# Kernel optimization log

Hardware: AMD Instinct MI355X
Metric: run time of the kernel (lower is better)

The kernel has to match this reference:

```python
import jax, jax.numpy as jnp
import numpy as np

B = 4          # graphs
N = 8192       # coarse nodes (2048/graph)
M = 65536      # fine (skip) nodes (16384/graph)
E = 131072     # edges (32768/graph)
T = 16         # global tokens per graph
F_IN = 16      # dim of x and x_skip (concat -> in_channels = 32)
HID, OUT = 32, 16
ED, GD, EMB, H = 3, 1024, 64, 4
K = 3


def _make_pe(t, d):
    # PositionalEncoding buffer (sin/cos), deterministic constant
    position = np.arange(t, dtype=np.float32)[:, None]
    div = np.exp(np.arange(0, d, 2, dtype=np.float32) * (-np.log(10000.0) / d))
    pe = np.zeros((t, d), dtype=np.float32)
    pe[:, 0::2] = np.sin(position * div)
    pe[:, 1::2] = np.cos(position * div)
    return jnp.asarray(pe)


def setup_inputs():
    key = jax.random.key(0)
    ks = jax.random.split(key, 30)
    n, m, e = N // B, M // B, E // B
    inp = {}
    inp['x'] = jax.random.normal(ks[0], (N, F_IN), jnp.float32)
    inp['pos'] = jax.random.normal(ks[1], (N, 3), jnp.float32)
    inp['batch'] = jnp.repeat(jnp.arange(B), n)
    inp['x_skip'] = jax.random.normal(ks[2], (M, F_IN), jnp.float32)
    inp['pos_skip'] = jax.random.normal(ks[3], (M, 3), jnp.float32)
    inp['batch_skip'] = jnp.repeat(jnp.arange(B), m)
    off = jnp.repeat(jnp.arange(B) * m, e)
    inp['edge_index'] = jax.random.randint(ks[4], (2, E), 0, m) + off[None, :]
    inp['global_token'] = jax.random.normal(ks[5], (B * T, GD), jnp.float32)
    def lin(k, o, i, s):
        return jax.random.normal(k, (o, i), jnp.float32) * s
    inp['Wq_w'] = lin(ks[6], EMB, ED, 0.3); inp['Wq_b'] = jnp.zeros((EMB,), jnp.float32)
    inp['Wk_w'] = lin(ks[7], EMB, GD, 0.03); inp['Wk_b'] = jnp.zeros((EMB,), jnp.float32)
    inp['Wv_w'] = lin(ks[8], EMB, GD, 0.03); inp['Wv_b'] = jnp.zeros((EMB,), jnp.float32)
    inp['in_proj_w'] = lin(ks[9], 3 * EMB, EMB, 0.125); inp['in_proj_b'] = jnp.zeros((3 * EMB,), jnp.float32)
    inp['out_w'] = lin(ks[10], EMB, EMB, 0.125); inp['out_b'] = jnp.zeros((EMB,), jnp.float32)
    dims = [(2 * F_IN, HID), (HID, HID), (HID, OUT)]
    for i, (ci, co) in enumerate(dims):
        inp[f'nn_w{i}'] = lin(ks[11 + 3 * i], ci * co, ED + EMB, 0.05)
        inp[f'nn_b{i}'] = jnp.zeros((ci * co,), jnp.float32)
        inp[f'root{i}'] = jax.random.normal(ks[12 + 3 * i], (ci, co), jnp.float32) * (1.0 / np.sqrt(ci))
        inp[f'bias{i}'] = jnp.zeros((co,), jnp.float32)
    return inp


def reference(x, pos, batch, x_skip, pos_skip, batch_skip, edge_index, global_token,
              Wq_w, Wq_b, Wk_w, Wk_b, Wv_w, Wv_b, in_proj_w, in_proj_b, out_w, out_b,
              nn_w0, nn_b0, root0, bias0, nn_w1, nn_b1, root1, bias1, nn_w2, nn_b2, root2, bias2):
    # ---- knn_interpolate (k=3, inverse squared-distance weighting) ----
    # graphs are equal-sized by construction so per-graph knn == batched knn
    pos_b = pos.reshape(B, -1, 3)
    posk_b = pos_skip.reshape(B, -1, 3)
    d2 = ((posk_b ** 2).sum(-1)[:, :, None] + (pos_b ** 2).sum(-1)[:, None, :]
          - 2.0 * jnp.einsum('bmc,bnc->bmn', posk_b, pos_b))  # [B,m,n]
    neg, idx = jax.lax.top_k(-d2, K)                           # [B,m,K]
    w = 1.0 / jnp.maximum(-neg, 1e-16)
    x_b = x.reshape(B, -1, x.shape[-1])
    feats = jnp.take_along_axis(x_b[:, None, :, :], idx[:, :, :, None], axis=2)  # [B,m,K,F]
    xf = ((w[..., None] * feats).sum(2) / w.sum(2)[..., None]).reshape(M, -1)

    src, dst = edge_index[0], edge_index[1]
    pseudo = pos_skip[dst] - pos_skip[src]                     # patch_size is None
    edge_pos = (0.5 * (pos_skip[dst] + pos_skip[src])).reshape(B, -1, 3)
    gt = global_token.reshape(B, -1, global_token.shape[-1])
    pe = _make_pe(gt.shape[1], EMB)
    Q = edge_pos @ Wq_w.T + Wq_b                               # [B,Eb,EMB]
    Kt = gt @ Wk_w.T + Wk_b + pe                               # dropout in eval = identity
    Vt = gt @ Wv_w.T + Wv_b + pe
    # ---- MultiheadAttention (batch_first) ----
    wq, wk, wv = jnp.split(in_proj_w, 3, axis=0)
    bq, bk, bv = jnp.split(in_proj_b, 3, axis=0)
    hd = EMB // H
    def heads(t, w_, b_):
        t = t @ w_.T + b_
        return t.reshape(t.shape[0], t.shape[1], H, hd).transpose(0, 2, 1, 3)
    q, k_, v = heads(Q, wq, bq), heads(Kt, wk, bk), heads(Vt, wv, bv)
    att = jax.nn.softmax(jnp.einsum('bhqd,bhkd->bhqk', q, k_) / np.sqrt(hd).astype(np.float32), axis=-1)
    o = jnp.einsum('bhqk,bhkd->bhqd', att, v).transpose(0, 2, 1, 3).reshape(B, -1, EMB)
    o = o @ out_w.T + out_b
    pseudo = jnp.concatenate([pseudo, o.reshape(-1, EMB)], axis=-1)  # [E, 3+64]

    # ---- NNConv stack (gather -> edge MLP -> per-edge matmul -> scatter mean) ----
    h = jnp.concatenate([xf, x_skip], axis=1)                  # [M, 32]
    ones = jnp.ones((E,), jnp.float32)
    cnt = jnp.maximum(jax.ops.segment_sum(ones, dst, num_segments=M), 1.0)[:, None]
    for nw, nb, rt, bs in ((nn_w0, nn_b0, root0, bias0),
                           (nn_w1, nn_b1, root1, bias1),
                           (nn_w2, nn_b2, root2, bias2)):
        ci, co = rt.shape
        we = jax.nn.relu(pseudo @ nw.T + nb).reshape(E, ci, co)  # MLP (BN at default eval stats ~ identity)
        msg = jnp.einsum('ei,eio->eo', h[src], we)               # [E, co]
        aggr = jax.ops.segment_sum(msg, dst, num_segments=M) / cnt
        h = jax.nn.relu(aggr + h @ rt + bs)                      # drop_act=False -> relu every layer
    return h, pos_skip, batch_skip
```

## Files before the change

### kernel.cpp

```cpp
#include <hip/hip_runtime.h>
#include <math.h>

#define NB    4
#define NN    8192
#define MM    65536
#define EE    131072
#define NPG   2048

typedef short short8 __attribute__((ext_vector_type(8)));
typedef float f32x4  __attribute__((ext_vector_type(4)));

static __device__ inline unsigned short f2b(float f) {
    unsigned u = __float_as_uint(f);
    u += 0x7fffu + ((u >> 16) & 1u);
    return (unsigned short)(u >> 16);
}
static __device__ inline unsigned f2b_pack(float a, float b) {
    unsigned x = __float_as_uint(a); x += 0x7fffu + ((x >> 16) & 1u);
    unsigned y = __float_as_uint(b); y += 0x7fffu + ((y >> 16) & 1u);
    return (x >> 16) | (y & 0xffff0000u);
}
static __device__ inline short8 bc8(uint4 v) {
    union { uint4 u; short8 s; } c; c.u = v; return c.s;
}

__global__ __launch_bounds__(512)
void k_knn(const float4* __restrict__ cpre, const float* __restrict__ pos_skip,
           const float* __restrict__ x, const float* __restrict__ x_skip,
           const int* __restrict__ batch_skip,
           float* __restrict__ h0, float* __restrict__ out_pos,
           float* __restrict__ out_batch)
{
    __shared__ float4 cp[2048];
    __shared__ float  pk[8][128][3];
    __shared__ int    chosen[128][3];
    __shared__ unsigned long long fin[3][128][3];
    __shared__ float  wFin[128][3];
    __shared__ int    iFin[128][3];

    int tid = threadIdx.x;
    int g = blockIdx.x >> 7;
    int cbase = g * NPG;
    int fbase = blockIdx.x * 128;
    int wave = tid >> 6;
    int lane = tid & 63;

    for (int c = tid; c < 2048; c += 512) cp[c] = cpre[cbase + c];

    int nA = lane, nB = lane + 64;
    float fxA = pos_skip[(fbase + nA) * 3 + 0];
    float fyA = pos_skip[(fbase + nA) * 3 + 1];
    float fzA = pos_skip[(fbase + nA) * 3 + 2];
    float fxB = pos_skip[(fbase + nB) * 3 + 0];
    float fyB = pos_skip[(fbase + nB) * 3 + 1];
    float fzB = pos_skip[(fbase + nB) * 3 + 2];
    __syncthreads();

    const float4* cps = cp + wave * 256;
    float k0A = 3.4028235e38f, k1A = 3.4028235e38f, k2A = 3.4028235e38f;
    float k0B = 3.4028235e38f, k1B = 3.4028235e38f, k2B = 3.4028235e38f;
#pragma unroll
    for (int j = 0; j < 8; ++j) {
        float mA = 3.4028235e38f, mB = 3.4028235e38f;
#pragma unroll 8
        for (int i = 0; i < 32; ++i) {
            float4 cc = cps[j * 32 + i];
            float dA = fmaf(cc.x, fxA, cc.w);
            dA = fmaf(cc.y, fyA, dA);
            dA = fmaf(cc.z, fzA, dA);
            mA = fminf(mA, dA);
            float dB = fmaf(cc.x, fxB, cc.w);
            dB = fmaf(cc.y, fyB, dB);
            dB = fmaf(cc.z, fzB, dB);
            mB = fminf(mB, dB);
        }
        unsigned cid = (unsigned)(wave * 8 + j);
        float keyA = __uint_as_float((__float_as_uint(mA) & 0xFFFFFFC0u) | cid);
        float tA = fmaxf(k1A, keyA);
        k2A = fminf(k2A, tA);
        k1A = __builtin_amdgcn_fmed3f(k0A, k1A, keyA);
        k0A = fminf(k0A, keyA);
        float keyB = __uint_as_float((__float_as_uint(mB) & 0xFFFFFFC0u) | cid);
        float tB = fmaxf(k1B, keyB);
        k2B = fminf(k2B, tB);
        k1B = __builtin_amdgcn_fmed3f(k0B, k1B, keyB);
        k0B = fminf(k0B, keyB);
    }
    pk[wave][nA][0] = k0A; pk[wave][nA][1] = k1A; pk[wave][nA][2] = k2A;
    pk[wave][nB][0] = k0B; pk[wave][nB][1] = k1B; pk[wave][nB][2] = k2B;
    __syncthreads();

    if (tid < 128) {
        int n = tid;
        float m0 = 3.4028235e38f, m1 = 3.4028235e38f, m2 = 3.4028235e38f;
#pragma unroll
        for (int s = 0; s < 8; ++s)
#pragma unroll
            for (int r = 0; r < 3; ++r) {
                float k = pk[s][n][r];
                float t = fmaxf(m1, k);
                m2 = fminf(m2, t);
                m1 = __builtin_amdgcn_fmed3f(m0, m1, k);
                m0 = fminf(m0, k);
            }
        chosen[n][0] = (int)(__float_as_uint(m0) & 63u);
        chosen[n][1] = (int)(__float_as_uint(m1) & 63u);
        chosen[n][2] = (int)(__float_as_uint(m2) & 63u);
    }
    __syncthreads();

    if ((tid >> 7) < 3) {
        int n = tid & 127;
        int j = tid >> 7;
        int cid = chosen[n][j];
        int fn = fbase + n;
        float gx = pos_skip[fn * 3 + 0], gy = pos_skip[fn * 3 + 1], gz = pos_skip[fn * 3 + 2];
        float gq = gx * gx + gy * gy + gz * gz;
        unsigned long long m0 = ~0ull, m1 = ~0ull, m2 = ~0ull;
#pragma unroll 4
        for (int i = 0; i < 32; ++i) {
            int ii = (i + lane) & 31;
            float4 cc = cp[cid * 32 + ii];
            float d = gq + cc.w;
            d = fmaf(cc.x, gx, d);
            d = fmaf(cc.y, gy, d);
            d = fmaf(cc.z, gz, d);
            d = fmaxf(d, 0.f);
            unsigned c = (unsigned)(cbase + cid * 32 + ii);
            unsigned long long kk = ((unsigned long long)__float_as_uint(d) << 32) | c;
            unsigned long long t1 = m0 > kk ? m0 : kk; m0 = m0 < kk ? m0 : kk;
            unsigned long long t2 = m1 > t1 ? m1 : t1; m1 = m1 < t1 ? m1 : t1;
            m2 = m2 < t2 ? m2 : t2;
        }
        fin[j][n][0] = m0; fin[j][n][1] = m1; fin[j][n][2] = m2;
    }
    __syncthreads();

    if (tid < 128) {
        int n = tid;
        int fn = fbase + n;
        unsigned long long m0 = ~0ull, m1 = ~0ull, m2 = ~0ull;
#pragma unroll
        for (int j = 0; j < 3; ++j)
#pragma unroll
            for (int r = 0; r < 3; ++r) {
                unsigned long long kk = fin[j][n][r];
                unsigned long long t1 = m0 > kk ? m0 : kk; m0 = m0 < kk ? m0 : kk;
                unsigned long long t2 = m1 > t1 ? m1 : t1; m1 = m1 < t1 ? m1 : t1;
                m2 = m2 < t2 ? m2 : t2;
            }
        float d0 = __uint_as_float((unsigned)(m0 >> 32));
        float d1 = __uint_as_float((unsigned)(m1 >> 32));
        float d2 = __uint_as_float((unsigned)(m2 >> 32));
        float w0 = 1.f / fmaxf(d0, 1e-16f);
        float w1 = 1.f / fmaxf(d1, 1e-16f);
        float w2 = 1.f / fmaxf(d2, 1e-16f);
        float inv = 1.f / (w0 + w1 + w2);
        wFin[n][0] = w0 * inv; wFin[n][1] = w1 * inv; wFin[n][2] = w2 * inv;
        iFin[n][0] = (int)(m0 & 0xffffffffull);
        iFin[n][1] = (int)(m1 & 0xffffffffull);
        iFin[n][2] = (int)(m2 & 0xffffffffull);
        float gx = pos_skip[fn * 3 + 0], gy = pos_skip[fn * 3 + 1], gz = pos_skip[fn * 3 + 2];
        out_pos[fn * 3 + 0] = gx; out_pos[fn * 3 + 1] = gy; out_pos[fn * 3 + 2] = gz;
        out_batch[fn] = (float)batch_skip[fn];
    }
    __syncthreads();

    int n2 = tid >> 2, part = tid & 3;
    int f2 = fbase + n2;
    float4* h04 = (float4*)(h0 + (size_t)f2 * 32);
    if (part < 2) {
        const float4* x4 = (const float4*)x;
        float w0 = wFin[n2][0], w1 = wFin[n2][1], w2 = wFin[n2][2];
        int a0 = iFin[n2][0] * 4, a1 = iFin[n2][1] * 4, a2 = iFin[n2][2] * 4;
#pragma unroll
        for (int j = 0; j < 2; ++j) {
            int cj = part * 2 + j;
            float4 v0 = x4[a0 + cj], v1 = x4[a1 + cj], v2 = x4[a2 + cj];
            float4 r;
            r.x = w0 * v0.x + w1 * v1.x + w2 * v2.x;
            r.y = w0 * v0.y + w1 * v1.y + w2 * v2.y;
            r.z = w0 * v0.z + w1 * v1.z + w2 * v2.z;
            r.w = w0 * v0.w + w1 * v1.w + w2 * v2.w;
            h04[cj] = r;
        }
    } else {
        const float4* xs4 = (const float4*)x_skip;
#pragma unroll
        for (int j = 0; j < 2; ++j) {
            int cj = (part - 2) * 2 + j;
            h04[4 + cj] = xs4[f2 * 4 + cj];
        }
    }
}

__global__ __launch_bounds__(128)
void k_tokens1(const float* __restrict__ gt,
               const float* __restrict__ Wk_w, const float* __restrict__ Wk_b,
               const float* __restrict__ Wv_w, const float* __restrict__ Wv_b,
               const float* __restrict__ pos, float4* __restrict__ cpre,
               float* __restrict__ KtVt)
{
    int cgid = blockIdx.x * 128 + threadIdx.x;
    {
        float px = pos[cgid * 3 + 0];
        float py = pos[cgid * 3 + 1];
        float pz = pos[cgid * 3 + 2];
        cpre[cgid] = make_float4(-2.f * px, -2.f * py, -2.f * pz,
                                 px * px + py * py + pz * pz);
    }
    int b = blockIdx.x >> 4;
    int t = blockIdx.x & 15;
    int which = threadIdx.x >> 6;
    int d = threadIdx.x & 63;
    const float* W = which ? Wv_w : Wk_w;
    const float* bias = which ? Wv_b : Wk_b;
    const float4* row = (const float4*)(gt + (size_t)(b * 16 + t) * 1024);
    const float4* wr = (const float4*)(W + (size_t)d * 1024);
    float acc = 0.f;
    for (int c = 0; c < 256; ++c) {
        float4 a = row[c], w = wr[c];
        acc += a.x * w.x; acc += a.y * w.y; acc += a.z * w.z; acc += a.w * w.w;
    }
    int i2 = d >> 1;
    float dv = expf((float)(2 * i2) * (-0.14391156831212787f));
    float ang = (float)t * dv;
    float pe = (d & 1) ? cosf(ang) : sinf(ang);
    KtVt[((size_t)(b * 2 + which) * 16 + t) * 64 + d] = acc + bias[d] + pe;
}

__global__ __launch_bounds__(256)
void k_tokens2(const float* __restrict__ KtVt,
               const float* __restrict__ in_proj_w, const float* __restrict__ in_proj_b,
               const float* __restrict__ out_w,
               const float* __restrict__ Wq_w, const float* __restrict__ Wq_b,
               float* __restrict__ Mfold, uint4* __restrict__ v2fG)
{
    int b = blockIdx.x;
    int tid = threadIdx.x;
    __shared__ float KtL[1024], VtL[1024], vv[1024], kproj[1024];
    __shared__ float v2L[4096];
    __shared__ float qWs[192], qbs[64];
    for (int idx = tid; idx < 1024; idx += 256) {
        KtL[idx] = KtVt[(size_t)(b * 2 + 0) * 1024 + idx];
        VtL[idx] = KtVt[(size_t)(b * 2 + 1) * 1024 + idx];
    }
    __syncthreads();
    for (int idx = tid; idx < 2048; idx += 256) {
        int which = idx >> 10; int td = idx & 1023; int t = td >> 6; int j = td & 63;
        int r = (which ? 128 : 64) + j;
        const float* w = in_proj_w + (size_t)r * 64;
        const float* src = which ? VtL : KtL;
        float acc = in_proj_b[r];
#pragma unroll 8
        for (int dd = 0; dd < 64; ++dd) acc += src[t * 64 + dd] * w[dd];
        if (which) vv[t * 64 + j] = acc;
        else kproj[t * 64 + j] = acc;
    }
    for (int idx = tid; idx < 192; idx += 256) {
        int c = idx >> 6; int j = idx & 63;
        float acc = 0.f;
        for (int dd = 0; dd < 64; ++dd) acc += in_proj_w[(size_t)j * 64 + dd] * Wq_w[dd * 3 + c];
        qWs[c * 64 + j] = acc;
    }
    for (int j = tid; j < 64; j += 256) {
        float acc = in_proj_b[j];
        for (int dd = 0; dd < 64; ++dd) acc += in_proj_w[(size_t)j * 64 + dd] * Wq_b[dd];
        qbs[j] = acc;
    }
    __syncthreads();
    for (int idx = tid; idx < 4096; idx += 256) {
        int jo = idx & 63; int th2 = idx >> 6; int h = th2 & 3; int t = th2 >> 2;
        float acc = 0.f;
#pragma unroll
        for (int dd = 0; dd < 16; ++dd)
            acc += vv[t * 64 + h * 16 + dd] * out_w[(size_t)jo * 64 + h * 16 + dd];
        v2L[(t * 4 + h) * 64 + jo] = acc;
    }
    {
        int th = tid >> 2, c = tid & 3;
        int t = th >> 2, h = th & 3;
        float acc = 0.f;
#pragma unroll
        for (int dd = h * 16; dd < h * 16 + 16; ++dd) {
            float w = (c == 0) ? qWs[dd] : (c == 1) ? qWs[64 + dd]
                    : (c == 2) ? qWs[128 + dd] : qbs[dd];
            acc += w * kproj[t * 64 + dd];
        }
        Mfold[((size_t)b * 64 + th) * 4 + c] = 0.25f * acc;
    }
    __syncthreads();
    for (int it = tid; it < 512; it += 256) {
        int lane = it & 63, fi = it >> 6;
        int mi = fi >> 1, step = fi & 1;
        int outd = mi * 16 + (lane & 15);
        int th0 = step * 32 + (lane >> 4) * 8;
        uint4 v;
        v.x = f2b_pack(v2L[(th0 + 0) * 64 + outd], v2L[(th0 + 1) * 64 + outd]);
        v.y = f2b_pack(v2L[(th0 + 2) * 64 + outd], v2L[(th0 + 3) * 64 + outd]);
        v.z = f2b_pack(v2L[(th0 + 4) * 64 + outd], v2L[(th0 + 5) * 64 + outd]);
        v.w = f2b_pack(v2L[(th0 + 6) * 64 + outd], v2L[(th0 + 7) * 64 + outd]);
        v2fG[((size_t)b * 8 + fi) * 64 + lane] = v;
    }
}

__global__ __launch_bounds__(256)
void k_edge_attn(const float* __restrict__ ps, const int* __restrict__ ei,
                 const float* __restrict__ Mfold, const uint4* __restrict__ v2f,
                 const float* __restrict__ ob,
                 unsigned short* __restrict__ Pf, float* __restrict__ cnt)
{
    __shared__ unsigned attL[4 * 64 * 34];
    int tid = threadIdx.x;
    int wave = tid >> 6, lane = tid & 63, q = lane >> 4, c15 = lane & 15;
    int g = blockIdx.x >> 7;
    int e = blockIdx.x * 256 + tid;
    int s = ei[e], d = ei[EE + e];
    atomicAdd(&cnt[d], 1.f);
    float sx = ps[s * 3], sy = ps[s * 3 + 1], sz = ps[s * 3 + 2];
    float dx = ps[d * 3], dy = ps[d * 3 + 1], dz = ps[d * 3 + 2];
    float px = dx - sx, py = dy - sy, pz = dz - sz;
    float ex = 0.5f * (dx + sx), ey = 0.5f * (dy + sy), ez = 0.5f * (dz + sz);

    const float4* Mg = (const float4*)Mfold + (size_t)g * 64;
    float sc[64];
#pragma unroll
    for (int th = 0; th < 64; ++th) {
        float4 m = Mg[th];
        sc[th] = ex * m.x + ey * m.y + ez * m.z + m.w;
    }
#pragma unroll
    for (int h = 0; h < 4; ++h) {
        float mx = sc[h];
#pragma unroll
        for (int t = 1; t < 16; ++t) mx = fmaxf(mx, sc[t * 4 + h]);
        float ssum = 0.f;
#pragma unroll
        for (int t = 0; t < 16; ++t) {
            float eo = expf(sc[t * 4 + h] - mx);
            sc[t * 4 + h] = eo; ssum += eo;
        }
        float inv = 1.f / ssum;
#pragma unroll
        for (int t = 0; t < 16; ++t) sc[t * 4 + h] *= inv;
    }
    unsigned* slab = attL + wave * 64 * 34;
#pragma unroll
    for (int k = 0; k < 16; ++k) {
        uint2 v;
        v.x = f2b_pack(sc[4 * k + 0], sc[4 * k + 1]);
        v.y = f2b_pack(sc[4 * k + 2], sc[4 * k + 3]);
        *(uint2*)&slab[lane * 34 + 2 * k] = v;
    }
    __syncthreads();

    uint4 v2a[4][2];
#pragma unroll
    for (int mi = 0; mi < 4; ++mi)
#pragma unroll
        for (int st = 0; st < 2; ++st)
            v2a[mi][st] = v2f[((size_t)g * 8 + mi * 2 + st) * 64 + lane];

    f32x4 acc[4][4];
#pragma unroll
    for (int mi = 0; mi < 4; ++mi)
#pragma unroll
        for (int nt = 0; nt < 4; ++nt) acc[mi][nt] = (f32x4){0.f, 0.f, 0.f, 0.f};

#pragma unroll
    for (int nt = 0; nt < 4; ++nt) {
        const unsigned* rb = &slab[(nt * 16 + c15) * 34];
        uint4 b0 = *(const uint4*)&rb[q * 4];
        uint4 b1 = *(const uint4*)&rb[16 + q * 4];
#pragma unroll
        for (int mi = 0; mi < 4; ++mi) {
            acc[mi][nt] = __builtin_amdgcn_mfma_f32_16x16x32_bf16(bc8(v2a[mi][0]), bc8(b0), acc[mi][nt], 0, 0, 0);
            acc[mi][nt] = __builtin_amdgcn_mfma_f32_16x16x32_bf16(bc8(v2a[mi][1]), bc8(b1), acc[mi][nt], 0, 0, 0);
        }
    }
    __syncthreads();

    float4 obv[4];
#pragma unroll
    for (int mi = 0; mi < 4; ++mi) obv[mi] = *(const float4*)(ob + mi * 16 + q * 4);
#pragma unroll
    for (int mi = 0; mi < 4; ++mi)
#pragma unroll
        for (int nt = 0; nt < 4; ++nt) {
            f32x4 a = acc[mi][nt];
            uint2 v;
            v.x = f2b_pack(a[0] + obv[mi].x, a[1] + obv[mi].y);
            v.y = f2b_pack(a[2] + obv[mi].z, a[3] + obv[mi].w);
            *(uint2*)&slab[(nt * 16 + c15) * 34 + mi * 8 + q * 2] = v;
        }
    __syncthreads();

    uint4* Pf4 = (uint4*)Pf;
#pragma unroll
    for (int et = 0; et < 4; ++et) {
        int etg = blockIdx.x * 16 + wave * 4 + et;
#pragma unroll
        for (int st = 0; st < 2; ++st) {
            uint4 w = *(const uint4*)&slab[(et * 16 + c15) * 34 + st * 16 + q * 4];
            Pf4[((size_t)etg * 3 + st) * 64 + lane] = w;
        }
    }
    int et2 = e >> 4, eL = e & 15;
    size_t tb = ((size_t)(et2 * 3 + 2) * 64 + 0 * 16 + eL) * 8;
    uint2 t0; t0.x = f2b_pack(px, py); t0.y = f2b_pack(pz, 1.0f);
    *(uint2*)(Pf + tb) = t0;
    uint2 z2; z2.x = 0u; z2.y = 0u;
    *(uint2*)(Pf + tb + 4) = z2;
#pragma unroll
    for (int quad = 1; quad < 4; ++quad) {
        size_t zb = ((size_t)(et2 * 3 + 2) * 64 + quad * 16 + eL) * 8;
        uint4 z4; z4.x = 0u; z4.y = 0u; z4.z = 0u; z4.w = 0u;
        *(uint4*)(Pf + zb) = z4;
    }
}

static __device__ inline void repack_one(const float* __restrict__ nw,
                                         const float* __restrict__ nb,
                                         unsigned short* __restrict__ Wf, int idx)
{
    int jj = idx & 7;
    int lane = (idx >> 3) & 63;
    int rest = idx >> 9;
    int s = rest % 3;
    int jt = rest / 3;
    int j = jt * 16 + (lane & 15);
    int k = s * 32 + (lane >> 4) * 8 + jj;
    float v;
    if (k < 64)       v = nw[(size_t)j * 67 + 3 + k];
    else if (k < 67)  v = nw[(size_t)j * 67 + (k - 64)];
    else if (k == 67) v = nb[j];
    else              v = 0.f;
    Wf[idx] = f2b(v);
}

__global__ __launch_bounds__(256)
void k_repackAll(const float* __restrict__ nw0, const float* __restrict__ nb0,
                 const float* __restrict__ nw1, const float* __restrict__ nb1,
                 const float* __restrict__ nw2, const float* __restrict__ nb2,
                 unsigned short* __restrict__ Wf0, unsigned short* __restrict__ Wf1,
                 unsigned short* __restrict__ Wf2)
{
    int idx = blockIdx.x * 256 + threadIdx.x;
    if (idx < 98304)        repack_one(nw0, nb0, Wf0, idx);
    else if (idx < 196608)  repack_one(nw1, nb1, Wf1, idx - 98304);
    else                    repack_one(nw2, nb2, Wf2, idx - 196608);
}

template<int CO>
__global__ __launch_bounds__(256, 4)
void k_conv_mfma(const uint4* __restrict__ Pf, const float* __restrict__ hin,
                 const int* __restrict__ ei, const uint4* __restrict__ Wf,
                 float* __restrict__ aggr)
{
    __shared__ float hL[128 * 36];
    __shared__ int sL[128];
    __shared__ int dL[128];
    constexpr int REDSZ = (CO == 16) ? 2 * 64 * 17 : 4;
    __shared__ float red[REDSZ];

    int tid = threadIdx.x;
    int e0 = blockIdx.x * 128;
    if (tid < 128) sL[tid] = ei[e0 + tid];
    else           dL[tid - 128] = ei[EE + e0 + (tid - 128)];
    __syncthreads();
    for (int idx = tid; idx < 1024; idx += 256) {
        int row = idx >> 3, c = idx & 7;
        const float4* hr = (const float4*)(hin + (size_t)sL[row] * 32);
        *(float4*)&hL[row * 36 + c * 4] = hr[c];
    }
    __syncthreads();

    int wave = tid >> 6, lane = tid & 63, quad = lane >> 4, col = lane & 15;
    int group = wave >> 1, half = wave & 1;

    uint4 a[4][3];
    int et0 = blockIdx.x * 8 + group * 4;
#pragma unroll
    for (int st = 0; st < 4; ++st)
#pragma unroll
        for (int s = 0; s < 3; ++s)
            a[st][s] = Pf[((size_t)(et0 + st) * 3 + s) * 64 + lane];

    float msg[4][4];
#pragma unroll
    for (int st = 0; st < 4; ++st)
#pragma unroll
        for (int r = 0; r < 4; ++r) msg[st][r] = 0.f;

    int ibase = (CO == 32) ? 0 : half * 16;
    constexpr int NI2 = (CO == 32) ? 16 : 8;

    for (int i2 = 0; i2 < NI2; ++i2) {
        float2 hv2[4][4];
#pragma unroll
        for (int st = 0; st < 4; ++st)
#pragma unroll
            for (int r = 0; r < 4; ++r)
                hv2[st][r] = *(const float2*)&hL[(group * 64 + st * 16 + quad * 4 + r) * 36
                                                 + ibase + i2 * 2];
#pragma unroll
        for (int ii = 0; ii < 2; ++ii) {
            int i = ibase + i2 * 2 + ii;
            int jt = (CO == 32) ? (i * 2 + half) : i;
            uint4 b0 = Wf[((size_t)jt * 3 + 0) * 64 + lane];
            uint4 b1 = Wf[((size_t)jt * 3 + 1) * 64 + lane];
            uint4 b2 = Wf[((size_t)jt * 3 + 2) * 64 + lane];
#pragma unroll
            for (int st = 0; st < 4; ++st) {
                f32x4 c = {0.f, 0.f, 0.f, 0.f};
                c = __builtin_amdgcn_mfma_f32_16x16x32_bf16(bc8(a[st][0]), bc8(b0), c, 0, 0, 0);
                c = __builtin_amdgcn_mfma_f32_16x16x32_bf16(bc8(a[st][1]), bc8(b1), c, 0, 0, 0);
                c = __builtin_amdgcn_mfma_f32_16x16x32_bf16(bc8(a[st][2]), bc8(b2), c, 0, 0, 0);
#pragma unroll
                for (int r = 0; r < 4; ++r) {
                    float hv = ii ? hv2[st][r].y : hv2[st][r].x;
                    msg[st][r] += hv * fmaxf(c[r], 0.f);
                }
            }
        }
    }

    if (CO == 32) {
#pragma unroll
        for (int st = 0; st < 4; ++st)
#pragma unroll
            for (int r = 0; r < 4; ++r) {
                int dv = dL[group * 64 + st * 16 + quad * 4 + r];
                atomicAdd(&aggr[(size_t)dv * 32 + half * 16 + col], msg[st][r]);
            }
    } else {
        if (half == 1) {
#pragma unroll
            for (int st = 0; st < 4; ++st)
#pragma unroll
                for (int r = 0; r < 4; ++r)
                    red[group * 64 * 17 + lane * 17 + st * 4 + r] = msg[st][r];
        }
        __syncthreads();
        if (half == 0) {
#pragma unroll
            for (int st = 0; st < 4; ++st)
#pragma unroll
                for (int r = 0; r < 4; ++r) {
                    float m = msg[st][r] + red[group * 64 * 17 + lane * 17 + st * 4 + r];
                    int dv = dL[group * 64 + st * 16 + quad * 4 + r];
                    atomicAdd(&aggr[(size_t)dv * 16 + col], m);
                }
        }
    }
}

template<int CO>
__global__ __launch_bounds__(256)
void k_update(float* __restrict__ aggr, const float* __restrict__ cnt,
              const float* __restrict__ hin, const float* __restrict__ root,
              const float* __restrict__ bias, float* __restrict__ hout)
{
    __shared__ float rL[32 * CO];
    __shared__ float bL[CO];
    int tid = threadIdx.x;
    for (int idx = tid; idx < 32 * CO; idx += 256) rL[idx] = root[idx];
    if (tid < CO) bL[tid] = bias[tid];
    __syncthreads();
    int gid = blockIdx.x * 256 + tid;
    int v = gid / CO;
    int o = gid % CO;
    float acc = aggr[gid] / fmaxf(cnt[v], 1.f) + bL[o];
    aggr[gid] = 0.f;
    const float* hr = hin + (size_t)v * 32;
#pragma unroll
    for (int i = 0; i < 32; ++i) acc += hr[i] * rL[i * CO + o];
    hout[gid] = fmaxf(acc, 0.f);
}

extern "C" void kernel_launch(void* const* d_in, const int* in_sizes, int n_in,
                              void* d_out, int out_size, void* d_ws, size_t ws_size,
                              hipStream_t stream)
{
    const float* x          = (const float*)d_in[0];
    const float* pos        = (const float*)d_in[1];
    const float* x_skip     = (const float*)d_in[3];
    const float* pos_skip   = (const float*)d_in[4];
    const int*   batch_skip = (const int*)  d_in[5];
    const int*   ei         = (const int*)  d_in[6];
    const float* gt         = (const float*)d_in[7];
    const float* Wq_w       = (const float*)d_in[8];
    const float* Wq_b       = (const float*)d_in[9];
    const float* Wk_w       = (const float*)d_in[10];
    const float* Wk_b       = (const float*)d_in[11];
    const float* Wv_w       = (const float*)d_in[12];
    const float* Wv_b       = (const float*)d_in[13];
    const float* in_proj_w  = (const float*)d_in[14];
    const float* in_proj_b  = (const float*)d_in[15];
    const float* out_w      = (const float*)d_in[16];
    const float* out_b      = (const float*)d_in[17];
    const float* nn_w0 = (const float*)d_in[18]; const float* nn_b0 = (const float*)d_in[19];
    const float* root0 = (const float*)d_in[20]; const float* bias0 = (const float*)d_in[21];
    const float* nn_w1 = (const float*)d_in[22]; const float* nn_b1 = (const float*)d_in[23];
    const float* root1 = (const float*)d_in[24]; const float* bias1 = (const float*)d_in[25];
    const float* nn_w2 = (const float*)d_in[26]; const float* nn_b2 = (const float*)d_in[27];
    const float* root2 = (const float*)d_in[28]; const float* bias2 = (const float*)d_in[29];

    char* wsb = (char*)d_ws;
    size_t off = 0;
    auto carve = [&](size_t bytes) { char* p = wsb + off; off += (bytes + 255) & ~(size_t)255; return p; };
    float* aggr = (float*)carve((size_t)MM * 32 * 4);
    float* cnt  = (float*)carve((size_t)MM * 4);
    float* hA   = (float*)carve((size_t)MM * 32 * 4);
    float* hB   = (float*)carve((size_t)MM * 32 * 4);
    unsigned short* Pf  = (unsigned short*)carve((size_t)EE * 96 * 2);
    unsigned short* Wf0 = (unsigned short*)carve((size_t)1024 * 96 * 2);
    unsigned short* Wf1 = (unsigned short*)carve((size_t)1024 * 96 * 2);
    unsigned short* Wf2 = (unsigned short*)carve((size_t)512 * 96 * 2);
    float* Mfold = (float*)carve((size_t)NB * 64 * 4 * 4);
    uint4* v2f   = (uint4*)carve((size_t)NB * 8 * 64 * 16);
    float* KtVt  = (float*)carve((size_t)NB * 2 * 16 * 64 * 4);
    float4* cpre = (float4*)carve((size_t)NN * 16);

    float* h_final   = (float*)d_out;
    float* out_pos   = (float*)d_out + (size_t)MM * 16;
    float* out_batch = (float*)d_out + (size_t)MM * 19;

    hipMemsetAsync(aggr, 0, ((size_t)MM * 32 + MM) * sizeof(float), stream);

    k_tokens1<<<64, 128, 0, stream>>>(gt, Wk_w, Wk_b, Wv_w, Wv_b, pos, cpre, KtVt);
    k_tokens2<<<NB, 256, 0, stream>>>(KtVt, in_proj_w, in_proj_b, out_w, Wq_w, Wq_b,
                                      Mfold, v2f);
    k_knn<<<MM / 128, 512, 0, stream>>>(cpre, pos_skip, x, x_skip, batch_skip,
                                        hA, out_pos, out_batch);
    k_edge_attn<<<EE / 256, 256, 0, stream>>>(pos_skip, ei, Mfold, v2f, out_b,
                                              Pf, cnt);
    k_repackAll<<<960, 256, 0, stream>>>(nn_w0, nn_b0, nn_w1, nn_b1, nn_w2, nn_b2,
                                         Wf0, Wf1, Wf2);

    k_conv_mfma<32><<<EE / 128, 256, 0, stream>>>((const uint4*)Pf, hA, ei, (const uint4*)Wf0, aggr);
    k_update<32><<<(MM * 32) / 256, 256, 0, stream>>>(aggr, cnt, hA, root0, bias0, hB);
    k_conv_mfma<32><<<EE / 128, 256, 0, stream>>>((const uint4*)Pf, hB, ei, (const uint4*)Wf1, aggr);
    k_update<32><<<(MM * 32) / 256, 256, 0, stream>>>(aggr, cnt, hB, root1, bias1, hA);
    k_conv_mfma<16><<<EE / 128, 256, 0, stream>>>((const uint4*)Pf, hA, ei, (const uint4*)Wf2, aggr);
    k_update<16><<<(MM * 16) / 256, 256, 0, stream>>>(aggr, cnt, hA, root2, bias2, h_final);
}
```

Measured before the change: 345.8 us.

## Transpose gathered node features in LDS and compute kNN prep inline

Result: slower. 354.1 us (+2.4%).

```diff
diff --git a/kernel.cpp b/kernel.cpp
--- a/kernel.cpp
+++ b/kernel.cpp
@@ -9,6 +9,7 @@
 
 typedef short short8 __attribute__((ext_vector_type(8)));
 typedef float f32x4  __attribute__((ext_vector_type(4)));
+typedef float f32x2  __attribute__((ext_vector_type(2)));
 
 static __device__ inline unsigned short f2b(float f) {
     unsigned u = __float_as_uint(f);
@@ -25,7 +26,7 @@
 }
 
 __global__ __launch_bounds__(512)
-void k_knn(const float4* __restrict__ cpre, const float* __restrict__ pos_skip,
+void k_knn(const float* __restrict__ pos, const float* __restrict__ pos_skip,
            const float* __restrict__ x, const float* __restrict__ x_skip,
            const int* __restrict__ batch_skip,
            float* __restrict__ h0, float* __restrict__ out_pos,
@@ -45,7 +46,14 @@
     int wave = tid >> 6;
     int lane = tid & 63;
 
-    for (int c = tid; c < 2048; c += 512) cp[c] = cpre[cbase + c];
+    for (int c = tid; c < 2048; c += 512) {
+        int cc = cbase + c;
+        float px = pos[cc * 3 + 0];
+        float py = pos[cc * 3 + 1];
+        float pz = pos[cc * 3 + 2];
+        cp[c] = make_float4(-2.f * px, -2.f * py, -2.f * pz,
+                            px * px + py * py + pz * pz);
+    }
 
     int nA = lane, nB = lane + 64;
     float fxA = pos_skip[(fbase + nA) * 3 + 0];
@@ -198,17 +206,8 @@
 void k_tokens1(const float* __restrict__ gt,
                const float* __restrict__ Wk_w, const float* __restrict__ Wk_b,
                const float* __restrict__ Wv_w, const float* __restrict__ Wv_b,
-               const float* __restrict__ pos, float4* __restrict__ cpre,
                float* __restrict__ KtVt)
 {
-    int cgid = blockIdx.x * 128 + threadIdx.x;
-    {
-        float px = pos[cgid * 3 + 0];
-        float py = pos[cgid * 3 + 1];
-        float pz = pos[cgid * 3 + 2];
-        cpre[cgid] = make_float4(-2.f * px, -2.f * py, -2.f * pz,
-                                 px * px + py * py + pz * pz);
-    }
     int b = blockIdx.x >> 4;
     int t = blockIdx.x & 15;
     int which = threadIdx.x >> 6;
@@ -457,7 +456,7 @@
                  const int* __restrict__ ei, const uint4* __restrict__ Wf,
                  float* __restrict__ aggr)
 {
-    __shared__ float hL[128 * 36];
+    __shared__ float hT[32 * 130];
     __shared__ int sL[128];
     __shared__ int dL[128];
     constexpr int REDSZ = (CO == 16) ? 2 * 64 * 17 : 4;
@@ -471,7 +470,11 @@
     for (int idx = tid; idx < 1024; idx += 256) {
         int row = idx >> 3, c = idx & 7;
         const float4* hr = (const float4*)(hin + (size_t)sL[row] * 32);
-        *(float4*)&hL[row * 36 + c * 4] = hr[c];
+        float4 v = hr[c];
+        hT[(c * 4 + 0) * 130 + row] = v.x;
+        hT[(c * 4 + 1) * 130 + row] = v.y;
+        hT[(c * 4 + 2) * 130 + row] = v.z;
+        hT[(c * 4 + 3) * 130 + row] = v.w;
     }
     __syncthreads();
 
@@ -486,71 +489,74 @@
         for (int s = 0; s < 3; ++s)
             a[st][s] = Pf[((size_t)(et0 + st) * 3 + s) * 64 + lane];
 
-    float msg[4][4];
-#pragma unroll
-    for (int st = 0; st < 4; ++st)
-#pragma unroll
-        for (int r = 0; r < 4; ++r) msg[st][r] = 0.f;
-
+    f32x2 msg[4][2];
+#pragma unroll
+    for (int st = 0; st < 4; ++st) {
+        msg[st][0] = (f32x2){0.f, 0.f};
+        msg[st][1] = (f32x2){0.f, 0.f};
+    }
+
+    int rowb = group * 64 + quad * 4;
     int ibase = (CO == 32) ? 0 : half * 16;
-    constexpr int NI2 = (CO == 32) ? 16 : 8;
-
-    for (int i2 = 0; i2 < NI2; ++i2) {
-        float2 hv2[4][4];
+    constexpr int NI = (CO == 32) ? 32 : 16;
+
+#pragma unroll 2
+    for (int io = 0; io < NI; ++io) {
+        int i = ibase + io;
+        int jt = (CO == 32) ? (i * 2 + half) : i;
+        uint4 b0 = Wf[((size_t)jt * 3 + 0) * 64 + lane];
+        uint4 b1 = Wf[((size_t)jt * 3 + 1) * 64 + lane];
+        uint4 b2 = Wf[((size_t)jt * 3 + 2) * 64 + lane];
+        const float* hTi = &hT[i * 130 + rowb];
+#pragma unroll
+        for (int st = 0; st < 4; ++st) {
+            f32x4 c4 = {0.f, 0.f, 0.f, 0.f};
+            c4 = __builtin_amdgcn_mfma_f32_16x16x32_bf16(bc8(a[st][0]), bc8(b0), c4, 0, 0, 0);
+            c4 = __builtin_amdgcn_mfma_f32_16x16x32_bf16(bc8(a[st][1]), bc8(b1), c4, 0, 0, 0);
+            c4 = __builtin_amdgcn_mfma_f32_16x16x32_bf16(bc8(a[st][2]), bc8(b2), c4, 0, 0, 0);
+            f32x2 h01 = *(const f32x2*)&hTi[st * 16 + 0];
+            f32x2 h23 = *(const f32x2*)&hTi[st * 16 + 2];
+            f32x2 r01; r01[0] = fmaxf(c4[0], 0.f); r01[1] = fmaxf(c4[1], 0.f);
+            f32x2 r23; r23[0] = fmaxf(c4[2], 0.f); r23[1] = fmaxf(c4[3], 0.f);
+            msg[st][0] += h01 * r01;
+            msg[st][1] += h23 * r23;
+        }
+    }
+
+    if (CO == 32) {
 #pragma unroll
         for (int st = 0; st < 4; ++st)
 #pragma unroll
-            for (int r = 0; r < 4; ++r)
-                hv2[st][r] = *(const float2*)&hL[(group * 64 + st * 16 + quad * 4 + r) * 36
-                                                 + ibase + i2 * 2];
-#pragma unroll
-        for (int ii = 0; ii < 2; ++ii) {
-            int i = ibase + i2 * 2 + ii;
-            int jt = (CO == 32) ? (i * 2 + half) : i;
-            uint4 b0 = Wf[((size_t)jt * 3 + 0) * 64 + lane];
-            uint4 b1 = Wf[((size_t)jt * 3 + 1) * 64 + lane];
-            uint4 b2 = Wf[((size_t)jt * 3 + 2) * 64 + lane];
-#pragma unroll
-            for (int st = 0; st < 4; ++st) {
-                f32x4 c = {0.f, 0.f, 0.f, 0.f};
-                c = __builtin_amdgcn_mfma_f32_16x16x32_bf16(bc8(a[st][0]), bc8(b0), c, 0, 0, 0);
-                c = __builtin_amdgcn_mfma_f32_16x16x32_bf16(bc8(a[st][1]), bc8(b1), c, 0, 0, 0);
-                c = __builtin_amdgcn_mfma_f32_16x16x32_bf16(bc8(a[st][2]), bc8(b2), c, 0, 0, 0);
-#pragma unroll
-                for (int r = 0; r < 4; ++r) {
-                    float hv = ii ? hv2[st][r].y : hv2[st][r].x;
-                    msg[st][r] += hv * fmaxf(c[r], 0.f);
+            for (int p = 0; p < 2; ++p)
+#pragma unroll
+                for (int e2 = 0; e2 < 2; ++e2) {
+                    int r = p * 2 + e2;
+                    int dv = dL[group * 64 + st * 16 + quad * 4 + r];
+                    atomicAdd(&aggr[(size_t)dv * 32 + half * 16 + col], msg[st][p][e2]);
                 }
-            }
-        }
-    }
-
-    if (CO == 32) {
-#pragma unroll
-        for (int st = 0; st < 4; ++st)
-#pragma unroll
-            for (int r = 0; r < 4; ++r) {
-                int dv = dL[group * 64 + st * 16 + quad * 4 + r];
-                atomicAdd(&aggr[(size_t)dv * 32 + half * 16 + col], msg[st][r]);
-            }
     } else {
         if (half == 1) {
 #pragma unroll
             for (int st = 0; st < 4; ++st)
 #pragma unroll
-                for (int r = 0; r < 4; ++r)
-                    red[group * 64 * 17 + lane * 17 + st * 4 + r] = msg[st][r];
+                for (int p = 0; p < 2; ++p)
+#pragma unroll
+                    for (int e2 = 0; e2 < 2; ++e2)
+                        red[group * 64 * 17 + lane * 17 + st * 4 + p * 2 + e2] = msg[st][p][e2];
         }
         __syncthreads();
         if (half == 0) {
 #pragma unroll
             for (int st = 0; st < 4; ++st)
 #pragma unroll
-                for (int r = 0; r < 4; ++r) {
-                    float m = msg[st][r] + red[group * 64 * 17 + lane * 17 + st * 4 + r];
-                    int dv = dL[group * 64 + st * 16 + quad * 4 + r];
-                    atomicAdd(&aggr[(size_t)dv * 16 + col], m);
-                }
+                for (int p = 0; p < 2; ++p)
+#pragma unroll
+                    for (int e2 = 0; e2 < 2; ++e2) {
+                        int r = p * 2 + e2;
+                        float m = msg[st][p][e2] + red[group * 64 * 17 + lane * 17 + st * 4 + r];
+                        int dv = dL[group * 64 + st * 16 + quad * 4 + r];
+                        atomicAdd(&aggr[(size_t)dv * 16 + col], m);
+                    }
         }
     }
 }
@@ -620,7 +626,6 @@
     float* Mfold = (float*)carve((size_t)NB * 64 * 4 * 4);
     uint4* v2f   = (uint4*)carve((size_t)NB * 8 * 64 * 16);
     float* KtVt  = (float*)carve((size_t)NB * 2 * 16 * 64 * 4);
-    float4* cpre = (float4*)carve((size_t)NN * 16);
 
     float* h_final   = (float*)d_out;
     float* out_pos   = (float*)d_out + (size_t)MM * 16;
@@ -628,11 +633,11 @@
 
     hipMemsetAsync(aggr, 0, ((size_t)MM * 32 + MM) * sizeof(float), stream);
 
-    k_tokens1<<<64, 128, 0, stream>>>(gt, Wk_w, Wk_b, Wv_w, Wv_b, pos, cpre, KtVt);
+    k_knn<<<MM / 128, 512, 0, stream>>>(pos, pos_skip, x, x_skip, batch_skip,
+                                        hA, out_pos, out_batch);
+    k_tokens1<<<64, 128, 0, stream>>>(gt, Wk_w, Wk_b, Wv_w, Wv_b, KtVt);
     k_tokens2<<<NB, 256, 0, stream>>>(KtVt, in_proj_w, in_proj_b, out_w, Wq_w, Wq_b,
                                       Mfold, v2f);
-    k_knn<<<MM / 128, 512, 0, stream>>>(cpre, pos_skip, x, x_skip, batch_skip,
-                                        hA, out_pos, out_batch);
     k_edge_attn<<<EE / 256, 256, 0, stream>>>(pos_skip, ei, Mfold, v2f, out_b,
                                               Pf, cnt);
     k_repackAll<<<960, 256, 0, stream>>>(nn_w0, nn_b0, nn_w1, nn_b1, nn_w2, nn_b2,
```

## Double edges per conv block to reuse weight loads; fold coarse prep into kNN

Applied to the files above, without the earlier changes.

Result: slower. 381.5 us (+10.3%).

```diff
diff --git a/kernel.cpp b/kernel.cpp
--- a/kernel.cpp
+++ b/kernel.cpp
@@ -9,6 +9,7 @@
 
 typedef short short8 __attribute__((ext_vector_type(8)));
 typedef float f32x4  __attribute__((ext_vector_type(4)));
+typedef float f32x2  __attribute__((ext_vector_type(2)));
 
 static __device__ inline unsigned short f2b(float f) {
     unsigned u = __float_as_uint(f);
@@ -25,7 +26,7 @@
 }
 
 __global__ __launch_bounds__(512)
-void k_knn(const float4* __restrict__ cpre, const float* __restrict__ pos_skip,
+void k_knn(const float* __restrict__ pos, const float* __restrict__ pos_skip,
            const float* __restrict__ x, const float* __restrict__ x_skip,
            const int* __restrict__ batch_skip,
            float* __restrict__ h0, float* __restrict__ out_pos,
@@ -45,7 +46,14 @@
     int wave = tid >> 6;
     int lane = tid & 63;
 
-    for (int c = tid; c < 2048; c += 512) cp[c] = cpre[cbase + c];
+    for (int c = tid; c < 2048; c += 512) {
+        int cc = cbase + c;
+        float px = pos[cc * 3 + 0];
+        float py = pos[cc * 3 + 1];
+        float pz = pos[cc * 3 + 2];
+        cp[c] = make_float4(-2.f * px, -2.f * py, -2.f * pz,
+                            px * px + py * py + pz * pz);
+    }
 
     int nA = lane, nB = lane + 64;
     float fxA = pos_skip[(fbase + nA) * 3 + 0];
@@ -198,17 +206,8 @@
 void k_tokens1(const float* __restrict__ gt,
                const float* __restrict__ Wk_w, const float* __restrict__ Wk_b,
                const float* __restrict__ Wv_w, const float* __restrict__ Wv_b,
-               const float* __restrict__ pos, float4* __restrict__ cpre,
                float* __restrict__ KtVt)
 {
-    int cgid = blockIdx.x * 128 + threadIdx.x;
-    {
-        float px = pos[cgid * 3 + 0];
-        float py = pos[cgid * 3 + 1];
-        float pz = pos[cgid * 3 + 2];
-        cpre[cgid] = make_float4(-2.f * px, -2.f * py, -2.f * pz,
-                                 px * px + py * py + pz * pz);
-    }
     int b = blockIdx.x >> 4;
     int t = blockIdx.x & 15;
     int which = threadIdx.x >> 6;
@@ -452,23 +451,23 @@
 }
 
 template<int CO>
-__global__ __launch_bounds__(256, 4)
+__global__ __launch_bounds__(256, 2)
 void k_conv_mfma(const uint4* __restrict__ Pf, const float* __restrict__ hin,
                  const int* __restrict__ ei, const uint4* __restrict__ Wf,
                  float* __restrict__ aggr)
 {
-    __shared__ float hL[128 * 36];
-    __shared__ int sL[128];
-    __shared__ int dL[128];
-    constexpr int REDSZ = (CO == 16) ? 2 * 64 * 17 : 4;
+    __shared__ float hL[256 * 36];
+    __shared__ int sL[256];
+    __shared__ int dL[256];
+    constexpr int REDSZ = (CO == 16) ? 2 * 64 * 33 : 4;
     __shared__ float red[REDSZ];
 
     int tid = threadIdx.x;
-    int e0 = blockIdx.x * 128;
-    if (tid < 128) sL[tid] = ei[e0 + tid];
-    else           dL[tid - 128] = ei[EE + e0 + (tid - 128)];
-    __syncthreads();
-    for (int idx = tid; idx < 1024; idx += 256) {
+    int e0 = blockIdx.x * 256;
+    sL[tid] = ei[e0 + tid];
+    dL[tid] = ei[EE + e0 + tid];
+    __syncthreads();
+    for (int idx = tid; idx < 2048; idx += 256) {
         int row = idx >> 3, c = idx & 7;
         const float4* hr = (const float4*)(hin + (size_t)sL[row] * 32);
         *(float4*)&hL[row * 36 + c * 4] = hr[c];
@@ -478,31 +477,32 @@
     int wave = tid >> 6, lane = tid & 63, quad = lane >> 4, col = lane & 15;
     int group = wave >> 1, half = wave & 1;
 
-    uint4 a[4][3];
-    int et0 = blockIdx.x * 8 + group * 4;
-#pragma unroll
-    for (int st = 0; st < 4; ++st)
+    uint4 a[8][3];
+    int et0 = blockIdx.x * 16 + group * 8;
+#pragma unroll
+    for (int st = 0; st < 8; ++st)
 #pragma unroll
         for (int s = 0; s < 3; ++s)
             a[st][s] = Pf[((size_t)(et0 + st) * 3 + s) * 64 + lane];
 
-    float msg[4][4];
-#pragma unroll
-    for (int st = 0; st < 4; ++st)
+    float msg[8][4];
+#pragma unroll
+    for (int st = 0; st < 8; ++st)
 #pragma unroll
         for (int r = 0; r < 4; ++r) msg[st][r] = 0.f;
 
+    int rowb = group * 128 + quad * 4;
     int ibase = (CO == 32) ? 0 : half * 16;
     constexpr int NI2 = (CO == 32) ? 16 : 8;
 
     for (int i2 = 0; i2 < NI2; ++i2) {
-        float2 hv2[4][4];
-#pragma unroll
-        for (int st = 0; st < 4; ++st)
+        f32x2 hv2[8][4];
+#pragma unroll
+        for (int st = 0; st < 8; ++st)
 #pragma unroll
             for (int r = 0; r < 4; ++r)
-                hv2[st][r] = *(const float2*)&hL[(group * 64 + st * 16 + quad * 4 + r) * 36
-                                                 + ibase + i2 * 2];
+                hv2[st][r] = *(const f32x2*)&hL[(rowb + st * 16 + r) * 36
+                                                + ibase + i2 * 2];
 #pragma unroll
         for (int ii = 0; ii < 2; ++ii) {
             int i = ibase + i2 * 2 + ii;
@@ -511,14 +511,14 @@
             uint4 b1 = Wf[((size_t)jt * 3 + 1) * 64 + lane];
             uint4 b2 = Wf[((size_t)jt * 3 + 2) * 64 + lane];
 #pragma unroll
-            for (int st = 0; st < 4; ++st) {
+            for (int st = 0; st < 8; ++st) {
                 f32x4 c = {0.f, 0.f, 0.f, 0.f};
                 c = __builtin_amdgcn_mfma_f32_16x16x32_bf16(bc8(a[st][0]), bc8(b0), c, 0, 0, 0);
                 c = __builtin_amdgcn_mfma_f32_16x16x32_bf16(bc8(a[st][1]), bc8(b1), c, 0, 0, 0);
                 c = __builtin_amdgcn_mfma_f32_16x16x32_bf16(bc8(a[st][2]), bc8(b2), c, 0, 0, 0);
 #pragma unroll
                 for (int r = 0; r < 4; ++r) {
-                    float hv = ii ? hv2[st][r].y : hv2[st][r].x;
+                    float hv = ii ? hv2[st][r][1] : hv2[st][r][0];
                     msg[st][r] += hv * fmaxf(c[r], 0.f);
                 }
             }
@@ -527,28 +527,28 @@
 
     if (CO == 32) {
 #pragma unroll
-        for (int st = 0; st < 4; ++st)
+        for (int st = 0; st < 8; ++st)
 #pragma unroll
             for (int r = 0; r < 4; ++r) {
-                int dv = dL[group * 64 + st * 16 + quad * 4 + r];
+                int dv = dL[rowb + st * 16 + r];
                 atomicAdd(&aggr[(size_t)dv * 32 + half * 16 + col], msg[st][r]);
             }
     } else {
         if (half == 1) {
 #pragma unroll
-            for (int st = 0; st < 4; ++st)
+            for (int st = 0; st < 8; ++st)
 #pragma unroll
                 for (int r = 0; r < 4; ++r)
-                    red[group * 64 * 17 + lane * 17 + st * 4 + r] = msg[st][r];
+                    red[group * 64 * 33 + lane * 33 + st * 4 + r] = msg[st][r];
         }
         __syncthreads();
         if (half == 0) {
 #pragma unroll
-            for (int st = 0; st < 4; ++st)
+            for (int st = 0; st < 8; ++st)
 #pragma unroll
                 for (int r = 0; r < 4; ++r) {
-                    float m = msg[st][r] + red[group * 64 * 17 + lane * 17 + st * 4 + r];
-                    int dv = dL[group * 64 + st * 16 + quad * 4 + r];
+                    float m = msg[st][r] + red[group * 64 * 33 + lane * 33 + st * 4 + r];
+                    int dv = dL[rowb + st * 16 + r];
                     atomicAdd(&aggr[(size_t)dv * 16 + col], m);
                 }
         }
@@ -620,7 +620,6 @@
     float* Mfold = (float*)carve((size_t)NB * 64 * 4 * 4);
     uint4* v2f   = (uint4*)carve((size_t)NB * 8 * 64 * 16);
     float* KtVt  = (float*)carve((size_t)NB * 2 * 16 * 64 * 4);
-    float4* cpre = (float4*)carve((size_t)NN * 16);
 
     float* h_final   = (float*)d_out;
     float* out_pos   = (float*)d_out + (size_t)MM * 16;
@@ -628,20 +627,20 @@
 
     hipMemsetAsync(aggr, 0, ((size_t)MM * 32 + MM) * sizeof(float), stream);
 
-    k_tokens1<<<64, 128, 0, stream>>>(gt, Wk_w, Wk_b, Wv_w, Wv_b, pos, cpre, KtVt);
+    k_knn<<<MM / 128, 512, 0, stream>>>(pos, pos_skip, x, x_skip, batch_skip,
+                                        hA, out_pos, out_batch);
+    k_tokens1<<<64, 128, 0, stream>>>(gt, Wk_w, Wk_b, Wv_w, Wv_b, KtVt);
     k_tokens2<<<NB, 256, 0, stream>>>(KtVt, in_proj_w, in_proj_b, out_w, Wq_w, Wq_b,
                                       Mfold, v2f);
-    k_knn<<<MM / 128, 512, 0, stream>>>(cpre, pos_skip, x, x_skip, batch_skip,
-                                        hA, out_pos, out_batch);
     k_edge_attn<<<EE / 256, 256, 0, stream>>>(pos_skip, ei, Mfold, v2f, out_b,
                                               Pf, cnt);
     k_repackAll<<<960, 256, 0, stream>>>(nn_w0, nn_b0, nn_w1, nn_b1, nn_w2, nn_b2,
                                          Wf0, Wf1, Wf2);
 
-    k_conv_mfma<32><<<EE / 128, 256, 0, stream>>>((const uint4*)Pf, hA, ei, (const uint4*)Wf0, aggr);
+    k_conv_mfma<32><<<EE / 256, 256, 0, stream>>>((const uint4*)Pf, hA, ei, (const uint4*)Wf0, aggr);
     k_update<32><<<(MM * 32) / 256, 256, 0, stream>>>(aggr, cnt, hA, root0, bias0, hB);
-    k_conv_mfma<32><<<EE / 128, 256, 0, stream>>>((const uint4*)Pf, hB, ei, (const uint4*)Wf1, aggr);
+    k_conv_mfma<32><<<EE / 256, 256, 0, stream>>>((const uint4*)Pf, hB, ei, (const uint4*)Wf1, aggr);
     k_update<32><<<(MM * 32) / 256, 256, 0, stream>>>(aggr, cnt, hB, root1, bias1, hA);
-    k_conv_mfma<16><<<EE / 128, 256, 0, stream>>>((const uint4*)Pf, hA, ei, (const uint4*)Wf2, aggr);
+    k_conv_mfma<16><<<EE / 256, 256, 0, stream>>>((const uint4*)Pf, hA, ei, (const uint4*)Wf2, aggr);
     k_update<16><<<(MM * 16) / 256, 256, 0, stream>>>(aggr, cnt, hA, root2, bias2, h_final);
 }
```

## Split conv input-channel loop across two blocks and fold coarse precompute into kNN

Applied to the files above, without the earlier changes.

Result: slower. 517.9 us (+49.8%).

```diff
diff --git a/kernel.cpp b/kernel.cpp
--- a/kernel.cpp
+++ b/kernel.cpp
@@ -9,6 +9,7 @@
 
 typedef short short8 __attribute__((ext_vector_type(8)));
 typedef float f32x4  __attribute__((ext_vector_type(4)));
+typedef float f32x2  __attribute__((ext_vector_type(2)));
 
 static __device__ inline unsigned short f2b(float f) {
     unsigned u = __float_as_uint(f);
@@ -25,7 +26,7 @@
 }
 
 __global__ __launch_bounds__(512)
-void k_knn(const float4* __restrict__ cpre, const float* __restrict__ pos_skip,
+void k_knn(const float* __restrict__ pos, const float* __restrict__ pos_skip,
            const float* __restrict__ x, const float* __restrict__ x_skip,
            const int* __restrict__ batch_skip,
            float* __restrict__ h0, float* __restrict__ out_pos,
@@ -45,7 +46,14 @@
     int wave = tid >> 6;
     int lane = tid & 63;
 
-    for (int c = tid; c < 2048; c += 512) cp[c] = cpre[cbase + c];
+    for (int c = tid; c < 2048; c += 512) {
+        int cc = cbase + c;
+        float px = pos[cc * 3 + 0];
+        float py = pos[cc * 3 + 1];
+        float pz = pos[cc * 3 + 2];
+        cp[c] = make_float4(-2.f * px, -2.f * py, -2.f * pz,
+                            px * px + py * py + pz * pz);
+    }
 
     int nA = lane, nB = lane + 64;
     float fxA = pos_skip[(fbase + nA) * 3 + 0];
@@ -198,17 +206,8 @@
 void k_tokens1(const float* __restrict__ gt,
                const float* __restrict__ Wk_w, const float* __restrict__ Wk_b,
                const float* __restrict__ Wv_w, const float* __restrict__ Wv_b,
-               const float* __restrict__ pos, float4* __restrict__ cpre,
                float* __restrict__ KtVt)
 {
-    int cgid = blockIdx.x * 128 + threadIdx.x;
-    {
-        float px = pos[cgid * 3 + 0];
-        float py = pos[cgid * 3 + 1];
-        float pz = pos[cgid * 3 + 2];
-        cpre[cgid] = make_float4(-2.f * px, -2.f * py, -2.f * pz,
-                                 px * px + py * py + pz * pz);
-    }
     int b = blockIdx.x >> 4;
     int t = blockIdx.x & 15;
     int which = threadIdx.x >> 6;
@@ -452,7 +451,7 @@
 }
 
 template<int CO>
-__global__ __launch_bounds__(256, 4)
+__global__ __launch_bounds__(256, 5)
 void k_conv_mfma(const uint4* __restrict__ Pf, const float* __restrict__ hin,
                  const int* __restrict__ ei, const uint4* __restrict__ Wf,
                  float* __restrict__ aggr)
@@ -464,7 +463,9 @@
     __shared__ float red[REDSZ];
 
     int tid = threadIdx.x;
-    int e0 = blockIdx.x * 128;
+    int et = blockIdx.x & 1023;
+    int ih = blockIdx.x >> 10;
+    int e0 = et * 128;
     if (tid < 128) sL[tid] = ei[e0 + tid];
     else           dL[tid - 128] = ei[EE + e0 + (tid - 128)];
     __syncthreads();
@@ -479,7 +480,7 @@
     int group = wave >> 1, half = wave & 1;
 
     uint4 a[4][3];
-    int et0 = blockIdx.x * 8 + group * 4;
+    int et0 = et * 8 + group * 4;
 #pragma unroll
     for (int st = 0; st < 4; ++st)
 #pragma unroll
@@ -492,8 +493,8 @@
 #pragma unroll
         for (int r = 0; r < 4; ++r) msg[st][r] = 0.f;
 
-    int ibase = (CO == 32) ? 0 : half * 16;
-    constexpr int NI2 = (CO == 32) ? 16 : 8;
+    int ibase = (CO == 32) ? ih * 16 : ih * 16 + half * 8;
+    constexpr int NI2 = (CO == 32) ? 8 : 4;
 
     for (int i2 = 0; i2 < NI2; ++i2) {
         float2 hv2[4][4];
@@ -620,7 +621,6 @@
     float* Mfold = (float*)carve((size_t)NB * 64 * 4 * 4);
     uint4* v2f   = (uint4*)carve((size_t)NB * 8 * 64 * 16);
     float* KtVt  = (float*)carve((size_t)NB * 2 * 16 * 64 * 4);
-    float4* cpre = (float4*)carve((size_t)NN * 16);
 
     float* h_final   = (float*)d_out;
     float* out_pos   = (float*)d_out + (size_t)MM * 16;
@@ -628,20 +628,20 @@
 
     hipMemsetAsync(aggr, 0, ((size_t)MM * 32 + MM) * sizeof(float), stream);
 
-    k_tokens1<<<64, 128, 0, stream>>>(gt, Wk_w, Wk_b, Wv_w, Wv_b, pos, cpre, KtVt);
+    k_knn<<<MM / 128, 512, 0, stream>>>(pos, pos_skip, x, x_skip, batch_skip,
+                                        hA, out_pos, out_batch);
+    k_tokens1<<<64, 128, 0, stream>>>(gt, Wk_w, Wk_b, Wv_w, Wv_b, KtVt);
     k_tokens2<<<NB, 256, 0, stream>>>(KtVt, in_proj_w, in_proj_b, out_w, Wq_w, Wq_b,
                                       Mfold, v2f);
-    k_knn<<<MM / 128, 512, 0, stream>>>(cpre, pos_skip, x, x_skip, batch_skip,
-                                        hA, out_pos, out_batch);
     k_edge_attn<<<EE / 256, 256, 0, stream>>>(pos_skip, ei, Mfold, v2f, out_b,
                                               Pf, cnt);
     k_repackAll<<<960, 256, 0, stream>>>(nn_w0, nn_b0, nn_w1, nn_b1, nn_w2, nn_b2,
                                          Wf0, Wf1, Wf2);
 
-    k_conv_mfma<32><<<EE / 128, 256, 0, stream>>>((const uint4*)Pf, hA, ei, (const uint4*)Wf0, aggr);
+    k_conv_mfma<32><<<2048, 256, 0, stream>>>((const uint4*)Pf, hA, ei, (const uint4*)Wf0, aggr);
     k_update<32><<<(MM * 32) / 256, 256, 0, stream>>>(aggr, cnt, hA, root0, bias0, hB);
-    k_conv_mfma<32><<<EE / 128, 256, 0, stream>>>((const uint4*)Pf, hB, ei, (const uint4*)Wf1, aggr);
+    k_conv_mfma<32><<<2048, 256, 0, stream>>>((const uint4*)Pf, hB, ei, (const uint4*)Wf1, aggr);
     k_update<32><<<(MM * 32) / 256, 256, 0, stream>>>(aggr, cnt, hB, root1, bias1, hA);
-    k_conv_mfma<16><<<EE / 128, 256, 0, stream>>>((const uint4*)Pf, hA, ei, (const uint4*)Wf2, aggr);
+    k_conv_mfma<16><<<2048, 256, 0, stream>>>((const uint4*)Pf, hA, ei, (const uint4*)Wf2, aggr);
     k_update<16><<<(MM * 16) / 256, 256, 0, stream>>>(aggr, cnt, hA, root2, bias2, h_final);
 }
```
